# Optimization experiments

Measured on AMD Instinct MI355X. Metric: run time of the kernel, lower is better.

The kernel has to match this reference:

```python
import jax, jax.numpy as jnp
import numpy as np

B, T, I, H, O = 1024, 512, 128, 256, 64


def setup_inputs() -> dict:
    key = jax.random.key(0)
    ks = jax.random.split(key, 12)
    def lin(k, shape, fan_in):
        return jax.random.uniform(k, shape, jnp.float32, -1.0, 1.0) / np.sqrt(fan_in)
    return {
        "x": jax.random.normal(ks[0], (B, T, I), jnp.float32),
        "h0": jnp.zeros((B, H), jnp.float32),
        # GRUCell params (gate order: r, z, n as in PyTorch)
        "W_ih": lin(ks[1], (3 * H, I), H),
        "b_ih": lin(ks[2], (3 * H,), H),
        "W_hh": lin(ks[3], (3 * H, H), H),
        "b_hh": lin(ks[4], (3 * H,), H),
        # input_transform Linear(I -> H)
        "Wt": lin(ks[5], (H, I), I),
        "bt": lin(ks[6], (H,), I),
        # output_proj Linear(H -> O)
        "Wo": lin(ks[7], (O, H), H),
        "bo": lin(ks[8], (O,), H),
        # gate_proj Linear(H -> O)
        "Wg": lin(ks[9], (O, H), H),
        "bg": lin(ks[10], (O,), H),
    }


def reference(x, h0, W_ih, b_ih, W_hh, b_hh, Wt, bt, Wo, bo, Wg, bg):
    # Precompute all input-side projections with big GEMMs (time-major for scan)
    xi = jnp.einsum("bti,gi->tbg", x, W_ih) + b_ih          # [T,B,3H]
    ti = jax.nn.silu(jnp.einsum("bti,hi->tbh", x, Wt) + bt)  # [T,B,H]

    def step(h, inp):
        xi_t, ti_t = inp
        hh = h @ W_hh.T + b_hh                               # [B,3H]
        xr, xz, xn = jnp.split(xi_t, 3, axis=-1)
        hr, hz, hn = jnp.split(hh, 3, axis=-1)
        r = jax.nn.sigmoid(xr + hr)
        z = jax.nn.sigmoid(xz + hz)
        n = jnp.tanh(xn + r * hn)
        h_new = (1.0 - z) * n + z * h
        proj = (h_new + ti_t) @ Wo.T + bo                    # [B,O]
        gate = jax.nn.sigmoid(h_new @ Wg.T + bg)             # [B,O]
        return h_new, proj * gate

    _, outs = jax.lax.scan(step, h0, (xi, ti))               # outs: [T,B,O]
    return jnp.mean(outs, axis=0)                            # [B,O]
```

## Files before the change

kernel.cpp:

```cpp
#include <hip/hip_runtime.h>
#include <hip/hip_bf16.h>


typedef __attribute__((ext_vector_type(8))) __bf16 bf16x8;
typedef __attribute__((ext_vector_type(4))) __bf16 bf16x4;
typedef __attribute__((ext_vector_type(4))) float f32x4;

#define MFMA(a, b, c) __builtin_amdgcn_mfma_f32_16x16x32_bf16(a, b, c, 0, 0, 0)

__device__ __forceinline__ float fsig(float v) {
  float e = __builtin_amdgcn_exp2f(v * -1.442695041f);
  return __builtin_amdgcn_rcpf(1.0f + e);
}
__device__ __forceinline__ float ftanh(float v) {
  float e = __builtin_amdgcn_exp2f(v * 2.885390082f);
  return 1.0f - 2.0f * __builtin_amdgcn_rcpf(1.0f + e);
}

#define O_WIN 0u
#define O_WHH 262144u
#define O_WO  655360u
#define O_WG  688128u
#define O_B1  720896u
#define O_H   724992u
#define O_ACC 1773568u
#define O_TIO 2035712u

__global__ void k1_prep(const float* __restrict__ Wih, const float* __restrict__ Wt,
                        const float* __restrict__ Whh, const float* __restrict__ Wo,
                        const float* __restrict__ Wg, const float* __restrict__ bih,
                        const float* __restrict__ bhh, const float* __restrict__ bt,
                        const float* __restrict__ h0, char* __restrict__ ws) {
  unsigned n = blockIdx.x * 256u + threadIdx.x;
  __bf16* win = (__bf16*)(ws + O_WIN);
  __bf16* whh = (__bf16*)(ws + O_WHH);
  __bf16* wo = (__bf16*)(ws + O_WO);
  __bf16* wg = (__bf16*)(ws + O_WG);
  float* b1 = (float*)(ws + O_B1);
  float* hb = (float*)(ws + O_H);
  float* ac = (float*)(ws + O_ACC);
  if (n < 98304u) win[n] = (__bf16)Wih[n];
  else if (n < 131072u) { unsigned i = n - 98304u; win[98304u + i] = (__bf16)Wt[i]; }
  else if (n < 327680u) { unsigned i = n - 131072u; whh[i] = (__bf16)Whh[i]; }
  else if (n < 344064u) { unsigned i = n - 327680u; wo[i] = (__bf16)Wo[i]; }
  else if (n < 360448u) { unsigned i = n - 344064u; wg[i] = (__bf16)Wg[i]; }
  else if (n < 361472u) {
    unsigned i = n - 360448u;
    float v = (i < 512u) ? (bih[i] + bhh[i]) : ((i < 768u) ? bih[i] : bt[i - 768u]);
    b1[i] = v;
  } else if (n < 623616u) { unsigned i = n - 361472u; hb[i] = h0[i]; }
  else if (n < 689152u) { unsigned i = n - 623616u; ac[i] = 0.0f; }
}

__global__ __launch_bounds__(256, 2) void k2_xi(
    const float* __restrict__ x, const __bf16* __restrict__ win,
    const float* __restrict__ b1, __bf16* __restrict__ xi, int t0, int tcbits) {
  extern __shared__ char sm2[];
  __bf16* Asm = (__bf16*)sm2;
  __bf16* Bsm = (__bf16*)(sm2 + 34816);
  const int tid = threadIdx.x;
  const int lane = tid & 63, wv = tid >> 6;
  const int m0 = blockIdx.x * 128;
  const int tcm = (1 << tcbits) - 1;
#pragma unroll
  for (int rnd = 0; rnd < 16; ++rnd) {
    int row = rnd * 8 + (tid >> 5);
    int cr = m0 + row;
    int bb = cr >> tcbits, tt = cr & tcm;
    const float* xr = x + ((size_t)bb * 512 + (size_t)(t0 + tt)) * 128 + (tid & 31) * 4;
    float4 v = *(const float4*)xr;
    bf16x4 b4 = {(__bf16)v.x, (__bf16)v.y, (__bf16)v.z, (__bf16)v.w};
    *(bf16x4*)&Asm[row * 136 + (tid & 31) * 4] = b4;
  }
  for (int nc = 0; nc < 6; ++nc) {
    __syncthreads();
#pragma unroll
    for (int rnd = 0; rnd < 8; ++rnd) {
      int rr = rnd * 16 + (tid >> 4);
      uint4 w4 = *(const uint4*)(win + (size_t)(nc * 128 + rr) * 128 + (tid & 15) * 8);
      *(uint4*)&Bsm[rr * 136 + (tid & 15) * 8] = w4;
    }
    __syncthreads();
    f32x4 zv = {0.f, 0.f, 0.f, 0.f};
    f32x4 acc[2][8];
#pragma unroll
    for (int mi = 0; mi < 2; ++mi)
#pragma unroll
      for (int nt = 0; nt < 8; ++nt) acc[mi][nt] = zv;
#pragma unroll
    for (int kt = 0; kt < 4; ++kt) {
      bf16x8 a0 = *(const bf16x8*)&Asm[(wv * 32 + (lane & 15)) * 136 + kt * 32 + (lane >> 4) * 8];
      bf16x8 a1 = *(const bf16x8*)&Asm[(wv * 32 + 16 + (lane & 15)) * 136 + kt * 32 + (lane >> 4) * 8];
#pragma unroll
      for (int nt = 0; nt < 8; ++nt) {
        bf16x8 b = *(const bf16x8*)&Bsm[(nt * 16 + (lane & 15)) * 136 + kt * 32 + (lane >> 4) * 8];
        acc[0][nt] = MFMA(a0, b, acc[0][nt]);
        acc[1][nt] = MFMA(a1, b, acc[1][nt]);
      }
    }
    __syncthreads();
#pragma unroll
    for (int nt = 0; nt < 8; ++nt) {
      float bv = b1[nc * 128 + nt * 16 + (lane & 15)];
#pragma unroll
      for (int mi = 0; mi < 2; ++mi)
#pragma unroll
        for (int r = 0; r < 4; ++r) {
          int rowb = wv * 32 + mi * 16 + (lane >> 4) * 4 + r;
          Bsm[rowb * 136 + nt * 16 + (lane & 15)] = (__bf16)(acc[mi][nt][r] + bv);
        }
    }
    __syncthreads();
#pragma unroll
    for (int rnd = 0; rnd < 8; ++rnd) {
      int row = rnd * 16 + (tid >> 4);
      int cr = m0 + row;
      int bb = cr >> tcbits, tt = cr & tcm;
      uint4 v = *(const uint4*)&Bsm[row * 136 + (tid & 15) * 8];
      *(uint4*)(xi + ((size_t)tt * 1024 + bb) * 768 + nc * 128 + (tid & 15) * 8) = v;
    }
  }
}

__global__ __launch_bounds__(256, 1) void k2_tio(
    const float* __restrict__ x, const __bf16* __restrict__ win,
    const __bf16* __restrict__ wo, const float* __restrict__ b1,
    const float* __restrict__ bo, __bf16* __restrict__ tio, int t0, int tcbits) {
  extern __shared__ char sm3[];
  __bf16* Asm = (__bf16*)sm3;
  __bf16* Bsm = (__bf16*)(sm3 + 34816);
  __bf16* Ti = (__bf16*)(sm3 + 69632);
  const int tid = threadIdx.x;
  const int lane = tid & 63, wv = tid >> 6;
  const int m0 = blockIdx.x * 128;
  const int tcm = (1 << tcbits) - 1;
#pragma unroll
  for (int rnd = 0; rnd < 16; ++rnd) {
    int row = rnd * 8 + (tid >> 5);
    int cr = m0 + row;
    int bb = cr >> tcbits, tt = cr & tcm;
    const float* xr = x + ((size_t)bb * 512 + (size_t)(t0 + tt)) * 128 + (tid & 31) * 4;
    float4 v = *(const float4*)xr;
    bf16x4 b4 = {(__bf16)v.x, (__bf16)v.y, (__bf16)v.z, (__bf16)v.w};
    *(bf16x4*)&Asm[row * 136 + (tid & 31) * 4] = b4;
  }
  for (int nc = 0; nc < 2; ++nc) {
    __syncthreads();
#pragma unroll
    for (int rnd = 0; rnd < 8; ++rnd) {
      int rr = rnd * 16 + (tid >> 4);
      uint4 w4 = *(const uint4*)(win + (size_t)(98304 / 128 + nc * 128 + rr) * 128 + (tid & 15) * 8);
      *(uint4*)&Bsm[rr * 136 + (tid & 15) * 8] = w4;
    }
    __syncthreads();
    f32x4 zv = {0.f, 0.f, 0.f, 0.f};
    f32x4 acc[2][8];
#pragma unroll
    for (int mi = 0; mi < 2; ++mi)
#pragma unroll
      for (int nt = 0; nt < 8; ++nt) acc[mi][nt] = zv;
#pragma unroll
    for (int kt = 0; kt < 4; ++kt) {
      bf16x8 a0 = *(const bf16x8*)&Asm[(wv * 32 + (lane & 15)) * 136 + kt * 32 + (lane >> 4) * 8];
      bf16x8 a1 = *(const bf16x8*)&Asm[(wv * 32 + 16 + (lane & 15)) * 136 + kt * 32 + (lane >> 4) * 8];
#pragma unroll
      for (int nt = 0; nt < 8; ++nt) {
        bf16x8 b = *(const bf16x8*)&Bsm[(nt * 16 + (lane & 15)) * 136 + kt * 32 + (lane >> 4) * 8];
        acc[0][nt] = MFMA(a0, b, acc[0][nt]);
        acc[1][nt] = MFMA(a1, b, acc[1][nt]);
      }
    }
#pragma unroll
    for (int nt = 0; nt < 8; ++nt) {
      float bv = b1[768 + nc * 128 + nt * 16 + (lane & 15)];
#pragma unroll
      for (int mi = 0; mi < 2; ++mi)
#pragma unroll
        for (int r = 0; r < 4; ++r) {
          int rowb = wv * 32 + mi * 16 + (lane >> 4) * 4 + r;
          float s = acc[mi][nt][r] + bv;
          s = s * __builtin_amdgcn_rcpf(1.0f + __builtin_amdgcn_exp2f(s * -1.442695041f));
          Ti[rowb * 264 + nc * 128 + nt * 16 + (lane & 15)] = (__bf16)s;
        }
    }
  }
  __syncthreads();
  for (int i = tid; i < 2048; i += 256) {
    int row = i >> 5;
    int c8 = (i & 31) * 8;
    *(uint4*)&Bsm[row * 264 + c8] = *(const uint4*)(wo + row * 256 + c8);
  }
  __syncthreads();
  f32x4 zv = {0.f, 0.f, 0.f, 0.f};
  f32x4 acc2[2][4];
#pragma unroll
  for (int mi = 0; mi < 2; ++mi)
#pragma unroll
    for (int nt = 0; nt < 4; ++nt) acc2[mi][nt] = zv;
#pragma unroll
  for (int kt = 0; kt < 8; ++kt) {
    bf16x8 a0 = *(const bf16x8*)&Ti[(wv * 32 + (lane & 15)) * 264 + kt * 32 + (lane >> 4) * 8];
    bf16x8 a1 = *(const bf16x8*)&Ti[(wv * 32 + 16 + (lane & 15)) * 264 + kt * 32 + (lane >> 4) * 8];
#pragma unroll
    for (int nt = 0; nt < 4; ++nt) {
      bf16x8 b = *(const bf16x8*)&Bsm[(nt * 16 + (lane & 15)) * 264 + kt * 32 + (lane >> 4) * 8];
      acc2[0][nt] = MFMA(a0, b, acc2[0][nt]);
      acc2[1][nt] = MFMA(a1, b, acc2[1][nt]);
    }
  }
#pragma unroll
  for (int nt = 0; nt < 4; ++nt) {
    int col = nt * 16 + (lane & 15);
    float bv = bo[col];
#pragma unroll
    for (int mi = 0; mi < 2; ++mi)
#pragma unroll
      for (int r = 0; r < 4; ++r) {
        int rowb = wv * 32 + mi * 16 + (lane >> 4) * 4 + r;
        int cr = m0 + rowb;
        int bb = cr >> tcbits, tt = cr & tcm;
        tio[((size_t)tt * 1024 + bb) * 64 + col] = (__bf16)(acc2[mi][nt][r] + bv);
      }
  }
}

__global__ __launch_bounds__(256, 1) void k3_rec(
    const __bf16* __restrict__ xi, const __bf16* __restrict__ tio,
    const __bf16* __restrict__ whh, const __bf16* __restrict__ wo,
    const __bf16* __restrict__ wg, const float* __restrict__ bhn,
    const float* __restrict__ bg, float* __restrict__ hbuf,
    float* __restrict__ accb, int TC) {
  extern __shared__ char sm[];
  __bf16* h_lds = (__bf16*)sm;
  float* pre = (float*)(sm + 8448);
  __bf16* xib = (__bf16*)(sm + 20736);
  __bf16* wow = (__bf16*)(sm + 34048);
  const int tid = threadIdx.x;
  const int lane = tid & 63, wv = tid >> 6;
  const int b0 = blockIdx.x * 4;
  const int gcp = lane * 4;

  bf16x8 wf[4][3][8];
#pragma unroll
  for (int p = 0; p < 4; ++p)
#pragma unroll
    for (int g = 0; g < 3; ++g)
#pragma unroll
      for (int kt = 0; kt < 8; ++kt) {
        int rowg = g * 256 + wv * 64 + p * 16 + (lane & 15);
        wf[p][g][kt] = *(const bf16x8*)(whh + (size_t)rowg * 256 + kt * 32 + (lane >> 4) * 8);
      }
  for (int i = tid; i < 4096; i += 256) {
    int row = i >> 5;
    int c8 = (i & 31) * 8;
    const __bf16* srcw = (row < 64) ? (wo + row * 256 + c8) : (wg + (row - 64) * 256 + c8);
    *(uint4*)&wow[row * 264 + c8] = *(const uint4*)srcw;
  }
  for (int i = tid; i < 2112; i += 256) ((unsigned*)h_lds)[i] = 0u;
  __syncthreads();
  float hreg[4];
  {
    f32x4 h4 = *(const f32x4*)(hbuf + (size_t)(b0 + wv) * 256 + gcp);
    hreg[0] = h4[0]; hreg[1] = h4[1]; hreg[2] = h4[2]; hreg[3] = h4[3];
    bf16x4 hb = {(__bf16)h4[0], (__bf16)h4[1], (__bf16)h4[2], (__bf16)h4[3]};
    *(bf16x4*)&h_lds[wv * 264 + gcp] = hb;
  }
  float bhnp[4];
#pragma unroll
  for (int p = 0; p < 4; ++p) bhnp[p] = bhn[wv * 64 + p * 16 + (lane & 15)];
  float bgv = bg[wv * 16 + (lane & 15)];
  float oacc[4] = {0.f, 0.f, 0.f, 0.f};
  if (lane < 16) {
#pragma unroll
    for (int r = 0; r < 4; ++r) oacc[r] = accb[(size_t)(b0 + r) * 64 + wv * 16 + lane];
  }
  {
    const uint2* s0 = (const uint2*)(xi + (size_t)b0 * 768);
    uint2* d0 = (uint2*)xib;
    d0[tid] = s0[tid]; d0[tid + 256] = s0[tid + 256]; d0[tid + 512] = s0[tid + 512];
    if (tid < 64) ((uint2*)(xib + 3072))[tid] = ((const uint2*)(tio + (size_t)b0 * 64))[tid];
  }
  __syncthreads();

#pragma unroll 1
  for (int t = 0; t < TC; ++t) {
    const int cur = t & 1, nxt = cur ^ 1;
    __bf16* xc = xib + cur * 3328;
    __bf16* xnb = xib + nxt * 3328;
    int tn = (t + 1 < TC) ? (t + 1) : t;
    uint2 pf0, pf1, pf2, pft;
    {
      const uint2* s = (const uint2*)(xi + ((size_t)tn * 1024 + b0) * 768);
      pf0 = s[tid]; pf1 = s[tid + 256]; pf2 = s[tid + 512];
      if (tid < 64) pft = ((const uint2*)(tio + ((size_t)tn * 1024 + b0) * 64))[tid];
    }
    bf16x8 afr[8];
#pragma unroll
    for (int kt = 0; kt < 8; ++kt)
      afr[kt] = *(const bf16x8*)&h_lds[(lane & 15) * 264 + kt * 32 + (lane >> 4) * 8];
#pragma unroll
    for (int p = 0; p < 4; ++p) {
      f32x4 ar = {0.f, 0.f, 0.f, 0.f}, az = {0.f, 0.f, 0.f, 0.f};
      f32x4 an = {bhnp[p], bhnp[p], bhnp[p], bhnp[p]};
#pragma unroll
      for (int kt = 0; kt < 8; ++kt) {
        ar = MFMA(afr[kt], wf[p][0][kt], ar);
        az = MFMA(afr[kt], wf[p][1][kt], az);
        an = MFMA(afr[kt], wf[p][2][kt], an);
      }
      if (lane < 16) {
        int col = wv * 64 + p * 16 + lane;
#pragma unroll
        for (int r = 0; r < 4; ++r) {
          pre[r * 256 + col] = ar[r];
          pre[1024 + r * 256 + col] = az[r];
          pre[2048 + r * 256 + col] = an[r];
        }
      }
    }
    __syncthreads();
    {
      f32x4 hr = *(const f32x4*)&pre[wv * 256 + gcp];
      f32x4 hz = *(const f32x4*)&pre[1024 + wv * 256 + gcp];
      f32x4 hn = *(const f32x4*)&pre[2048 + wv * 256 + gcp];
      bf16x4 xr4 = *(const bf16x4*)&xc[wv * 768 + gcp];
      bf16x4 xz4 = *(const bf16x4*)&xc[wv * 768 + 256 + gcp];
      bf16x4 xn4 = *(const bf16x4*)&xc[wv * 768 + 512 + gcp];
#pragma unroll
      for (int j = 0; j < 4; ++j) {
        float r = fsig((float)xr4[j] + hr[j]);
        float z = fsig((float)xz4[j] + hz[j]);
        float n = ftanh((float)xn4[j] + r * hn[j]);
        hreg[j] = n + z * (hreg[j] - n);
      }
      bf16x4 hb = {(__bf16)hreg[0], (__bf16)hreg[1], (__bf16)hreg[2], (__bf16)hreg[3]};
      *(bf16x4*)&h_lds[wv * 264 + gcp] = hb;
    }
    {
      uint2* d = (uint2*)xnb;
      d[tid] = pf0; d[tid + 256] = pf1; d[tid + 512] = pf2;
      if (tid < 64) ((uint2*)(xnb + 3072))[tid] = pft;
    }
    __syncthreads();
    {
      bf16x8 af2[8];
#pragma unroll
      for (int kt = 0; kt < 8; ++kt)
        af2[kt] = *(const bf16x8*)&h_lds[(lane & 15) * 264 + kt * 32 + (lane >> 4) * 8];
      f32x4 po = {0.f, 0.f, 0.f, 0.f};
      f32x4 pg = {bgv, bgv, bgv, bgv};
#pragma unroll
      for (int kt = 0; kt < 8; ++kt) {
        bf16x8 bfo = *(const bf16x8*)&wow[(wv * 16 + (lane & 15)) * 264 + kt * 32 + (lane >> 4) * 8];
        bf16x8 bfg = *(const bf16x8*)&wow[(64 + wv * 16 + (lane & 15)) * 264 + kt * 32 + (lane >> 4) * 8];
        po = MFMA(af2[kt], bfo, po);
        pg = MFMA(af2[kt], bfg, pg);
      }
      if (lane < 16) {
#pragma unroll
        for (int r = 0; r < 4; ++r) {
          float tv = (float)xc[3072 + r * 64 + wv * 16 + lane];
          float pov = po[r] + tv;
          float gv = fsig(pg[r]);
          oacc[r] += pov * gv;
        }
      }
    }
  }
  {
    f32x4 h4 = {hreg[0], hreg[1], hreg[2], hreg[3]};
    *(f32x4*)(hbuf + (size_t)(b0 + wv) * 256 + gcp) = h4;
  }
  if (lane < 16) {
#pragma unroll
    for (int r = 0; r < 4; ++r) accb[(size_t)(b0 + r) * 64 + wv * 16 + lane] = oacc[r];
  }
}

__global__ void k4_out(const float* __restrict__ accb, float* __restrict__ out) {
  int i = blockIdx.x * 256 + threadIdx.x;
  out[i] = accb[i] * (1.0f / 512.0f);
}

extern "C" void kernel_launch(void* const* d_in, const int* in_sizes, int n_in,
                              void* d_out, int out_size, void* d_ws, size_t ws_size,
                              hipStream_t stream) {
  const float* x = (const float*)d_in[0];
  const float* h0 = (const float*)d_in[1];
  const float* Wih = (const float*)d_in[2];
  const float* bih = (const float*)d_in[3];
  const float* Whh = (const float*)d_in[4];
  const float* bhh = (const float*)d_in[5];
  const float* Wt = (const float*)d_in[6];
  const float* bt = (const float*)d_in[7];
  const float* Wo = (const float*)d_in[8];
  const float* bo = (const float*)d_in[9];
  const float* Wg = (const float*)d_in[10];
  const float* bg = (const float*)d_in[11];
  float* out = (float*)d_out;
  char* ws = (char*)d_ws;

  int TC = 512;
  while (TC > 1 && (2035712ull + (size_t)TC * 1703936ull) > ws_size) TC >>= 1;
  int tcbits = 0;
  while ((1 << tcbits) != TC) ++tcbits;

  __bf16* win = (__bf16*)(ws + O_WIN);
  __bf16* whhb = (__bf16*)(ws + O_WHH);
  __bf16* wob = (__bf16*)(ws + O_WO);
  __bf16* wgb = (__bf16*)(ws + O_WG);
  float* b1 = (float*)(ws + O_B1);
  float* hbuf = (float*)(ws + O_H);
  float* accb = (float*)(ws + O_ACC);
  __bf16* tioc = (__bf16*)(ws + O_TIO);
  __bf16* xic = (__bf16*)(ws + O_TIO + (size_t)TC * 131072u);

  (void)hipFuncSetAttribute((const void*)k2_xi, hipFuncAttributeMaxDynamicSharedMemorySize, 69632);
  (void)hipFuncSetAttribute((const void*)k2_tio, hipFuncAttributeMaxDynamicSharedMemorySize, 137216);
  (void)hipFuncSetAttribute((const void*)k3_rec, hipFuncAttributeMaxDynamicSharedMemorySize, 101632);

  k1_prep<<<2692, 256, 0, stream>>>(Wih, Wt, Whh, Wo, Wg, bih, bhh, bt, h0, ws);
  int nch = 512 / TC;
  for (int c = 0; c < nch; ++c) {
    int t0 = c * TC;
    k2_xi<<<8 * TC, 256, 69632, stream>>>(x, win, b1, xic, t0, tcbits);
    k2_tio<<<8 * TC, 256, 137216, stream>>>(x, win, wob, b1, bo, tioc, t0, tcbits);
    k3_rec<<<256, 256, 101632, stream>>>(xic, tioc, whhb, wob, wgb, bhh + 512, bg, hbuf, accb, TC);
  }
  k4_out<<<256, 256, 0, stream>>>(accb, out);
}
```

Measured before the change: 2.214 ms.

## Split output projection out of recurrent loop into separate parallel kernel

The recurrent kernel now only computes the GRU hidden-state update, using 512 threads per block with gate math done directly in MFMA accumulator registers, and writes each step's hidden state to a history buffer in global memory. A new kernel then computes the output and gate projections plus the gated accumulation over time in parallel across timesteps, combining partial sums with atomics. This takes the per-step output GEMM and one barrier off the serial critical path, at the cost of extra global memory traffic for the hidden-state history and a larger workspace requirement, which may shrink the time chunk size.

```diff
diff --git a/kernel.cpp b/kernel.cpp
--- a/kernel.cpp
+++ b/kernel.cpp
@@ -224,157 +224,128 @@
   }
 }
 
-__global__ __launch_bounds__(256, 1) void k3_rec(
-    const __bf16* __restrict__ xi, const __bf16* __restrict__ tio,
-    const __bf16* __restrict__ whh, const __bf16* __restrict__ wo,
-    const __bf16* __restrict__ wg, const float* __restrict__ bhn,
-    const float* __restrict__ bg, float* __restrict__ hbuf,
-    float* __restrict__ accb, int TC) {
-  extern __shared__ char sm[];
-  __bf16* h_lds = (__bf16*)sm;
-  float* pre = (float*)(sm + 8448);
-  __bf16* xib = (__bf16*)(sm + 20736);
-  __bf16* wow = (__bf16*)(sm + 34048);
+__global__ __launch_bounds__(512, 2) void k3_rec(
+    const __bf16* __restrict__ xi, const __bf16* __restrict__ whh,
+    const float* __restrict__ bhn, float* __restrict__ hbuf,
+    __bf16* __restrict__ hhist, int TC) {
+  __shared__ __bf16 h_lds[2][4224];
   const int tid = threadIdx.x;
-  const int lane = tid & 63, wv = tid >> 6;
+  const int lane = tid & 63, w = tid >> 6;
+  const int ln = lane & 15, kg = lane >> 4;
   const int b0 = blockIdx.x * 4;
-  const int gcp = lane * 4;
-
-  bf16x8 wf[4][3][8];
-#pragma unroll
-  for (int p = 0; p < 4; ++p)
+
+  bf16x8 wf[2][3][8];
+#pragma unroll
+  for (int c = 0; c < 2; ++c)
 #pragma unroll
     for (int g = 0; g < 3; ++g)
 #pragma unroll
       for (int kt = 0; kt < 8; ++kt) {
-        int rowg = g * 256 + wv * 64 + p * 16 + (lane & 15);
-        wf[p][g][kt] = *(const bf16x8*)(whh + (size_t)rowg * 256 + kt * 32 + (lane >> 4) * 8);
-      }
-  for (int i = tid; i < 4096; i += 256) {
-    int row = i >> 5;
-    int c8 = (i & 31) * 8;
-    const __bf16* srcw = (row < 64) ? (wo + row * 256 + c8) : (wg + (row - 64) * 256 + c8);
-    *(uint4*)&wow[row * 264 + c8] = *(const uint4*)srcw;
-  }
-  for (int i = tid; i < 2112; i += 256) ((unsigned*)h_lds)[i] = 0u;
+        int rowg = g * 256 + w * 32 + c * 16 + ln;
+        wf[c][g][kt] = *(const bf16x8*)(whh + (size_t)rowg * 256 + kt * 32 + kg * 8);
+      }
+  for (int i = tid; i < 4224; i += 512) ((unsigned*)h_lds)[i] = 0u;
   __syncthreads();
-  float hreg[4];
-  {
-    f32x4 h4 = *(const f32x4*)(hbuf + (size_t)(b0 + wv) * 256 + gcp);
-    hreg[0] = h4[0]; hreg[1] = h4[1]; hreg[2] = h4[2]; hreg[3] = h4[3];
-    bf16x4 hb = {(__bf16)h4[0], (__bf16)h4[1], (__bf16)h4[2], (__bf16)h4[3]};
-    *(bf16x4*)&h_lds[wv * 264 + gcp] = hb;
-  }
-  float bhnp[4];
-#pragma unroll
-  for (int p = 0; p < 4; ++p) bhnp[p] = bhn[wv * 64 + p * 16 + (lane & 15)];
-  float bgv = bg[wv * 16 + (lane & 15)];
-  float oacc[4] = {0.f, 0.f, 0.f, 0.f};
-  if (lane < 16) {
-#pragma unroll
-    for (int r = 0; r < 4; ++r) oacc[r] = accb[(size_t)(b0 + r) * 64 + wv * 16 + lane];
-  }
-  {
-    const uint2* s0 = (const uint2*)(xi + (size_t)b0 * 768);
-    uint2* d0 = (uint2*)xib;
-    d0[tid] = s0[tid]; d0[tid + 256] = s0[tid + 256]; d0[tid + 512] = s0[tid + 512];
-    if (tid < 64) ((uint2*)(xib + 3072))[tid] = ((const uint2*)(tio + (size_t)b0 * 64))[tid];
+  float hm[2], bhnv[2];
+#pragma unroll
+  for (int c = 0; c < 2; ++c) {
+    int col = w * 32 + c * 16 + ln;
+    hm[c] = hbuf[(size_t)(b0 + kg) * 256 + col];
+    h_lds[0][(4 * kg) * 264 + col] = (__bf16)hm[c];
+    bhnv[c] = bhn[col];
   }
   __syncthreads();
+
+  const int voff = (b0 + kg) * 768 + w * 32 + ln;
 
 #pragma unroll 1
   for (int t = 0; t < TC; ++t) {
     const int cur = t & 1, nxt = cur ^ 1;
-    __bf16* xc = xib + cur * 3328;
-    __bf16* xnb = xib + nxt * 3328;
-    int tn = (t + 1 < TC) ? (t + 1) : t;
-    uint2 pf0, pf1, pf2, pft;
+    const __bf16* xt = xi + (size_t)t * 786432 + voff;
+    __bf16 pf[2][3];
+#pragma unroll
+    for (int c = 0; c < 2; ++c)
+#pragma unroll
+      for (int g = 0; g < 3; ++g) pf[c][g] = xt[g * 256 + c * 16];
+#pragma unroll
+    for (int c = 0; c < 2; ++c) {
+      f32x4 ar = {0.f, 0.f, 0.f, 0.f};
+      f32x4 az = {0.f, 0.f, 0.f, 0.f};
+      f32x4 an = {0.f, 0.f, 0.f, 0.f};
+#pragma unroll
+      for (int kt = 0; kt < 8; ++kt) {
+        bf16x8 a = *(const bf16x8*)&h_lds[cur][ln * 264 + kt * 32 + kg * 8];
+        ar = MFMA(a, wf[c][0][kt], ar);
+        az = MFMA(a, wf[c][1][kt], az);
+        an = MFMA(a, wf[c][2][kt], an);
+      }
+      float r = fsig((float)pf[c][0] + ar[0]);
+      float z = fsig((float)pf[c][1] + az[0]);
+      float n = ftanh((float)pf[c][2] + r * (an[0] + bhnv[c]));
+      hm[c] = n + z * (hm[c] - n);
+      h_lds[nxt][(4 * kg) * 264 + w * 32 + c * 16 + ln] = (__bf16)hm[c];
+    }
+    __syncthreads();
     {
-      const uint2* s = (const uint2*)(xi + ((size_t)tn * 1024 + b0) * 768);
-      pf0 = s[tid]; pf1 = s[tid + 256]; pf2 = s[tid + 512];
-      if (tid < 64) pft = ((const uint2*)(tio + ((size_t)tn * 1024 + b0) * 64))[tid];
-    }
-    bf16x8 afr[8];
-#pragma unroll
-    for (int kt = 0; kt < 8; ++kt)
-      afr[kt] = *(const bf16x8*)&h_lds[(lane & 15) * 264 + kt * 32 + (lane >> 4) * 8];
-#pragma unroll
-    for (int p = 0; p < 4; ++p) {
-      f32x4 ar = {0.f, 0.f, 0.f, 0.f}, az = {0.f, 0.f, 0.f, 0.f};
-      f32x4 an = {bhnp[p], bhnp[p], bhnp[p], bhnp[p]};
+      int row = tid >> 7, cd = tid & 127;
+      unsigned v = *(const unsigned*)&h_lds[nxt][(4 * row) * 264 + cd * 2];
+      *(unsigned*)(hhist + ((size_t)t * 1024 + b0 + row) * 256 + cd * 2) = v;
+    }
+  }
+#pragma unroll
+  for (int c = 0; c < 2; ++c)
+    hbuf[(size_t)(b0 + kg) * 256 + w * 32 + c * 16 + ln] = hm[c];
+}
+
+__global__ __launch_bounds__(256, 3) void k5_out(
+    const __bf16* __restrict__ hhist, const __bf16* __restrict__ tio,
+    const __bf16* __restrict__ wo, const __bf16* __restrict__ wg,
+    const float* __restrict__ bg, float* __restrict__ accb, int TC) {
+  const int tid = threadIdx.x;
+  const int lane = tid & 63, w = tid >> 6;
+  const int ln = lane & 15, kg = lane >> 4;
+  const int bt = blockIdx.x & 7;
+  const int t0 = (blockIdx.x >> 3) * 16;
+  bf16x8 bfo[8], bfg[8];
+#pragma unroll
+  for (int kt = 0; kt < 8; ++kt) {
+    bfo[kt] = *(const bf16x8*)(wo + (size_t)(w * 16 + ln) * 256 + kt * 32 + kg * 8);
+    bfg[kt] = *(const bf16x8*)(wg + (size_t)(w * 16 + ln) * 256 + kt * 32 + kg * 8);
+  }
+  float bgv = bg[w * 16 + ln];
+  f32x4 oacc[8];
+#pragma unroll
+  for (int m = 0; m < 8; ++m) oacc[m] = (f32x4){0.f, 0.f, 0.f, 0.f};
+#pragma unroll 1
+  for (int tt = 0; tt < 16; ++tt) {
+    int t = t0 + tt;
+    if (t >= TC) break;
+    const __bf16* hrow = hhist + ((size_t)t * 1024 + bt * 128) * 256;
+    const __bf16* trow = tio + ((size_t)t * 1024 + bt * 128) * 64;
+#pragma unroll
+    for (int m = 0; m < 8; ++m) {
+      f32x4 po = {0.f, 0.f, 0.f, 0.f};
+      f32x4 pg = {0.f, 0.f, 0.f, 0.f};
 #pragma unroll
       for (int kt = 0; kt < 8; ++kt) {
-        ar = MFMA(afr[kt], wf[p][0][kt], ar);
-        az = MFMA(afr[kt], wf[p][1][kt], az);
-        an = MFMA(afr[kt], wf[p][2][kt], an);
-      }
-      if (lane < 16) {
-        int col = wv * 64 + p * 16 + lane;
-#pragma unroll
-        for (int r = 0; r < 4; ++r) {
-          pre[r * 256 + col] = ar[r];
-          pre[1024 + r * 256 + col] = az[r];
-          pre[2048 + r * 256 + col] = an[r];
-        }
-      }
-    }
-    __syncthreads();
-    {
-      f32x4 hr = *(const f32x4*)&pre[wv * 256 + gcp];
-      f32x4 hz = *(const f32x4*)&pre[1024 + wv * 256 + gcp];
-      f32x4 hn = *(const f32x4*)&pre[2048 + wv * 256 + gcp];
-      bf16x4 xr4 = *(const bf16x4*)&xc[wv * 768 + gcp];
-      bf16x4 xz4 = *(const bf16x4*)&xc[wv * 768 + 256 + gcp];
-      bf16x4 xn4 = *(const bf16x4*)&xc[wv * 768 + 512 + gcp];
-#pragma unroll
-      for (int j = 0; j < 4; ++j) {
-        float r = fsig((float)xr4[j] + hr[j]);
-        float z = fsig((float)xz4[j] + hz[j]);
-        float n = ftanh((float)xn4[j] + r * hn[j]);
-        hreg[j] = n + z * (hreg[j] - n);
-      }
-      bf16x4 hb = {(__bf16)hreg[0], (__bf16)hreg[1], (__bf16)hreg[2], (__bf16)hreg[3]};
-      *(bf16x4*)&h_lds[wv * 264 + gcp] = hb;
-    }
-    {
-      uint2* d = (uint2*)xnb;
-      d[tid] = pf0; d[tid + 256] = pf1; d[tid + 512] = pf2;
-      if (tid < 64) ((uint2*)(xnb + 3072))[tid] = pft;
-    }
-    __syncthreads();
-    {
-      bf16x8 af2[8];
-#pragma unroll
-      for (int kt = 0; kt < 8; ++kt)
-        af2[kt] = *(const bf16x8*)&h_lds[(lane & 15) * 264 + kt * 32 + (lane >> 4) * 8];
-      f32x4 po = {0.f, 0.f, 0.f, 0.f};
-      f32x4 pg = {bgv, bgv, bgv, bgv};
-#pragma unroll
-      for (int kt = 0; kt < 8; ++kt) {
-        bf16x8 bfo = *(const bf16x8*)&wow[(wv * 16 + (lane & 15)) * 264 + kt * 32 + (lane >> 4) * 8];
-        bf16x8 bfg = *(const bf16x8*)&wow[(64 + wv * 16 + (lane & 15)) * 264 + kt * 32 + (lane >> 4) * 8];
-        po = MFMA(af2[kt], bfo, po);
-        pg = MFMA(af2[kt], bfg, pg);
-      }
-      if (lane < 16) {
-#pragma unroll
-        for (int r = 0; r < 4; ++r) {
-          float tv = (float)xc[3072 + r * 64 + wv * 16 + lane];
-          float pov = po[r] + tv;
-          float gv = fsig(pg[r]);
-          oacc[r] += pov * gv;
-        }
-      }
-    }
-  }
-  {
-    f32x4 h4 = {hreg[0], hreg[1], hreg[2], hreg[3]};
-    *(f32x4*)(hbuf + (size_t)(b0 + wv) * 256 + gcp) = h4;
-  }
-  if (lane < 16) {
-#pragma unroll
-    for (int r = 0; r < 4; ++r) accb[(size_t)(b0 + r) * 64 + wv * 16 + lane] = oacc[r];
-  }
+        bf16x8 a = *(const bf16x8*)(hrow + (size_t)(m * 16 + ln) * 256 + kt * 32 + kg * 8);
+        po = MFMA(a, bfo[kt], po);
+        pg = MFMA(a, bfg[kt], pg);
+      }
+#pragma unroll
+      for (int r = 0; r < 4; ++r) {
+        int row = m * 16 + kg * 4 + r;
+        float tv = (float)trow[row * 64 + w * 16 + ln];
+        oacc[m][r] += (po[r] + tv) * fsig(pg[r] + bgv);
+      }
+    }
+  }
+#pragma unroll
+  for (int m = 0; m < 8; ++m)
+#pragma unroll
+    for (int r = 0; r < 4; ++r)
+      atomicAdd(&accb[(size_t)(bt * 128 + m * 16 + kg * 4 + r) * 64 + w * 16 + ln],
+                oacc[m][r]);
 }
 
 __global__ void k4_out(const float* __restrict__ accb, float* __restrict__ out) {
@@ -401,7 +372,7 @@
   char* ws = (char*)d_ws;
 
   int TC = 512;
-  while (TC > 1 && (2035712ull + (size_t)TC * 1703936ull) > ws_size) TC >>= 1;
+  while (TC > 1 && (2035712ull + (size_t)TC * 2228224ull) > ws_size) TC >>= 1;
   int tcbits = 0;
   while ((1 << tcbits) != TC) ++tcbits;
 
@@ -413,11 +384,11 @@
   float* hbuf = (float*)(ws + O_H);
   float* accb = (float*)(ws + O_ACC);
   __bf16* tioc = (__bf16*)(ws + O_TIO);
-  __bf16* xic = (__bf16*)(ws + O_TIO + (size_t)TC * 131072u);
+  __bf16* hhist = (__bf16*)(ws + O_TIO + (size_t)TC * 131072u);
+  __bf16* xic = (__bf16*)(ws + O_TIO + (size_t)TC * 655360u);
 
   (void)hipFuncSetAttribute((const void*)k2_xi, hipFuncAttributeMaxDynamicSharedMemorySize, 69632);
   (void)hipFuncSetAttribute((const void*)k2_tio, hipFuncAttributeMaxDynamicSharedMemorySize, 137216);
-  (void)hipFuncSetAttribute((const void*)k3_rec, hipFuncAttributeMaxDynamicSharedMemorySize, 101632);
 
   k1_prep<<<2692, 256, 0, stream>>>(Wih, Wt, Whh, Wo, Wg, bih, bhh, bt, h0, ws);
   int nch = 512 / TC;
@@ -425,7 +396,9 @@
     int t0 = c * TC;
     k2_xi<<<8 * TC, 256, 69632, stream>>>(x, win, b1, xic, t0, tcbits);
     k2_tio<<<8 * TC, 256, 137216, stream>>>(x, win, wob, b1, bo, tioc, t0, tcbits);
-    k3_rec<<<256, 256, 101632, stream>>>(xic, tioc, whhb, wob, wgb, bhh + 512, bg, hbuf, accb, TC);
+    k3_rec<<<256, 512, 0, stream>>>(xic, whhb, bhh + 512, hbuf, hhist, TC);
+    int tch = (TC + 15) >> 4;
+    k5_out<<<8 * tch, 256, 0, stream>>>(hhist, tioc, wob, wgb, bg, accb, TC);
   }
   k4_out<<<256, 256, 0, stream>>>(accb, out);
 }
```

Measured after the change: 2.945 ms. 1.33x slower.
